# Optimization experiments

Measured on AMD Instinct MI355X. Metric: run time of the kernel, lower is better.

## Reference

```python
import jax, jax.numpy as jnp
import numpy as np

N, C, H, W = 4, 256, 64, 64
C_EMBED = C // 2  # 128

def setup_inputs() -> dict:
    key = jax.random.key(0)
    k1, k2, k3, k4 = jax.random.split(key, 4)
    x = jax.random.normal(k1, (N, C, H, W), dtype=jnp.float32)
    # 1x1 conv weights stored as [out_ch, in_ch] (torch Conv2d weight squeezed)
    theta_w = jax.random.normal(k2, (C_EMBED, C), dtype=jnp.float32) * 0.01
    phi_w = jax.random.normal(k3, (C_EMBED, C), dtype=jnp.float32) * 0.01
    proj_w = jax.random.normal(k4, (C, C), dtype=jnp.float32) * 0.01
    return {"x": x, "theta_w": theta_w, "phi_w": phi_w, "proj_w": proj_w}

def reference(x, theta_w, phi_w, proj_w):
    n, c, h, w = x.shape
    s = h * w
    xf = x.reshape(n, c, s)  # [n, c, s]
    theta = jnp.einsum('ec,ncs->nse', theta_w, xf)  # [n, s, e]
    phi = jnp.einsum('ec,ncs->nes', phi_w, xf)      # [n, e, s]
    scale = jnp.sqrt(jnp.float32(theta_w.shape[0]))
    f = jnp.einsum('nse,net->nst', theta, phi) / scale  # [n, s, s]
    f = jax.nn.softmax(f, axis=-1)
    y = jnp.einsum('nst,nct->ncs', f, xf)  # attend over g = x, -> [n, c, s]
    res = jnp.einsum('oc,ncs->nos', proj_w, y)  # 1x1 projection conv
    return x + res.reshape(n, c, h, w)
```

## Files before the change

kernel.cpp:

```cpp
#include <hip/hip_runtime.h>
#include <cstdint>
#include <cstddef>

#define NB 4
#define CH 256
#define SS 4096
#define EE 128
#define QSCALE 0.08838834764831845f

typedef __attribute__((ext_vector_type(8))) short bfrag;
typedef __attribute__((ext_vector_type(8))) unsigned short u16x8;
typedef __attribute__((ext_vector_type(4))) float f32x4;

__device__ __forceinline__ unsigned short f2bf(float f) {
  union { float f; unsigned int u; } v; v.f = f;
  unsigned int u = v.u;
  unsigned int r = u + 0x7FFFu + ((u >> 16) & 1u);
  return (unsigned short)(r >> 16);
}

__device__ __forceinline__ void lds_barrier() {
  asm volatile("s_waitcnt lgkmcnt(0)" ::: "memory");
  __builtin_amdgcn_s_barrier();
}

__global__ __launch_bounds__(256) void cvt_w(
    const float* __restrict__ thw, const float* __restrict__ phw,
    const float* __restrict__ pw,
    unsigned short* __restrict__ thwb, unsigned short* __restrict__ phwb,
    unsigned short* __restrict__ pwb)
{
  const int nw4 = EE * CH / 4;
  const int np4 = CH * CH / 4;
  int i = blockIdx.x * 256 + threadIdx.x;
  const float* src; unsigned short* dst; int off;
  if      (i < nw4)           { src = thw; dst = thwb; off = i; }
  else if (i < 2 * nw4)       { src = phw; dst = phwb; off = i - nw4; }
  else if (i < 2 * nw4 + np4) { src = pw;  dst = pwb;  off = i - 2 * nw4; }
  else return;
  float4 v = reinterpret_cast<const float4*>(src)[off];
  ushort4 o;
  o.x = f2bf(v.x); o.y = f2bf(v.y); o.z = f2bf(v.z); o.w = f2bf(v.w);
  reinterpret_cast<ushort4*>(dst)[off] = o;
}

__global__ __launch_bounds__(512) void pass1_qk(
    const float* __restrict__ x,
    const unsigned short* __restrict__ thw,
    const unsigned short* __restrict__ phw,
    unsigned short* __restrict__ xb,
    unsigned short* __restrict__ Qt,
    unsigned short* __restrict__ Kt)
{
  __shared__ unsigned short xT[64][CH + 8];
  const int t  = threadIdx.x;
  const int n  = blockIdx.y;
  const int s0 = blockIdx.x * 64;

  {
    const int soff = (t & 15) * 4;
    const int c0   = t >> 4;
    #pragma unroll
    for (int ci = 0; ci < 8; ++ci) {
      const int c = c0 + ci * 32;
      const size_t rowoff = ((size_t)n * CH + c) * SS + s0;
      float4 v = reinterpret_cast<const float4*>(x + rowoff)[soff >> 2];
      ushort4 o;
      o.x = f2bf(v.x); o.y = f2bf(v.y); o.z = f2bf(v.z); o.w = f2bf(v.w);
      reinterpret_cast<ushort4*>(xb + rowoff)[soff >> 2] = o;
      xT[soff + 0][c] = o.x;
      xT[soff + 1][c] = o.y;
      xT[soff + 2][c] = o.z;
      xT[soff + 3][c] = o.w;
    }
  }
  __syncthreads();

  const int w    = t >> 6;
  const int lane = t & 63;
  const int q    = lane >> 4;
  const int mr   = lane & 15;
  const int wrow = (w & 3) * 16;
  const int half = w >> 2;

  bfrag a[8];
  {
    const bfrag* rp = reinterpret_cast<const bfrag*>(&xT[wrow + mr][0]);
    #pragma unroll
    for (int k = 0; k < 8; ++k) a[k] = rp[k * 4 + q];
  }

  const unsigned short* wsel = half ? phw : thw;
  unsigned short*       osel = half ? Kt  : Qt;
  const float           sc   = half ? 1.0f : QSCALE;
  const bfrag* wp = reinterpret_cast<const bfrag*>(wsel);
  #pragma unroll
  for (int nt = 0; nt < 8; ++nt) {
    f32x4 acc = {0.f, 0.f, 0.f, 0.f};
    #pragma unroll
    for (int k = 0; k < 8; ++k) {
      bfrag b = wp[(nt * 16 + mr) * (CH / 8) + k * 4 + q];
      acc = __builtin_amdgcn_mfma_f32_16x16x32_bf16(a[k], b, acc, 0, 0, 0);
    }
    #pragma unroll
    for (int i = 0; i < 4; ++i) {
      const int srow = s0 + wrow + q * 4 + i;
      osel[((size_t)n * SS + srow) * EE + nt * 16 + mr] = f2bf(acc[i] * sc);
    }
  }
}

__global__ __launch_bounds__(512, 2) void pass2_attn(
    const unsigned short* __restrict__ Qt,
    const unsigned short* __restrict__ Kt,
    const unsigned short* __restrict__ xb,
    const unsigned short* __restrict__ pwb,
    const float* __restrict__ x,
    float* __restrict__ out)
{
  __shared__ __align__(16) unsigned char SMEM[51968];
  float          (*S_lds)[132] = reinterpret_cast<float(*)[132]>(SMEM);
  unsigned short (*P_lds)[136] = reinterpret_cast<unsigned short(*)[136]>(SMEM + 33792);
  float* row_m     = reinterpret_cast<float*>(SMEM + 51200);
  float* row_l     = reinterpret_cast<float*>(SMEM + 51456);
  float* row_alpha = reinterpret_cast<float*>(SMEM + 51712);

  const int t    = threadIdx.x;
  const int id   = blockIdx.x;
  const int xcd  = id & 7;
  const int n    = xcd >> 1;
  const int s0   = ((id >> 3) * 2 + (xcd & 1)) * 64;
  const int w    = t >> 6;
  const int lane = t & 63;
  const int q    = lane >> 4;
  const int mr   = lane & 15;

  if (t < 64) { row_m[t] = -INFINITY; row_l[t] = 0.f; }

  bfrag qa[4][4];
  #pragma unroll
  for (int ms = 0; ms < 4; ++ms) {
    const bfrag* rp = reinterpret_cast<const bfrag*>(
        Qt + ((size_t)n * SS + s0 + ms * 16 + mr) * EE);
    #pragma unroll
    for (int k = 0; k < 4; ++k) qa[ms][k] = rp[k * 4 + q];
  }

  f32x4 o_acc[4][2];
  #pragma unroll
  for (int ms = 0; ms < 4; ++ms)
    #pragma unroll
    for (int nt = 0; nt < 2; ++nt) o_acc[ms][nt] = (f32x4){0.f, 0.f, 0.f, 0.f};

  bfrag kb[4];
  {
    const bfrag* rp = reinterpret_cast<const bfrag*>(
        Kt + ((size_t)n * SS + w * 16 + mr) * EE);
    #pragma unroll
    for (int k = 0; k < 4; ++k) kb[k] = rp[k * 4 + q];
  }

  for (int t0 = 0; t0 < SS; t0 += 128) {
    bfrag vb[4][2];
    #pragma unroll
    for (int nt = 0; nt < 2; ++nt) {
      const int c = w * 32 + nt * 16 + mr;
      const bfrag* vp = reinterpret_cast<const bfrag*>(
          xb + ((size_t)n * CH + c) * SS + t0);
      #pragma unroll
      for (int kk = 0; kk < 4; ++kk) vb[kk][nt] = vp[kk * 4 + q];
    }

    #pragma unroll
    for (int ms = 0; ms < 4; ++ms) {
      f32x4 acc = {0.f, 0.f, 0.f, 0.f};
      #pragma unroll
      for (int k = 0; k < 4; ++k)
        acc = __builtin_amdgcn_mfma_f32_16x16x32_bf16(qa[ms][k], kb[k], acc, 0, 0, 0);
      #pragma unroll
      for (int i = 0; i < 4; ++i)
        S_lds[ms * 16 + q * 4 + i][w * 16 + mr] = acc[i];
    }
    lds_barrier();

    {
      const int t1 = t0 + 128;
      if (t1 < SS) {
        const bfrag* rp = reinterpret_cast<const bfrag*>(
            Kt + ((size_t)n * SS + t1 + w * 16 + mr) * EE);
        #pragma unroll
        for (int k = 0; k < 4; ++k) kb[k] = rp[k * 4 + q];
      }
    }

    {
      const int r  = t >> 3;
      const int cg = t & 7;
      const float4* srow = reinterpret_cast<const float4*>(&S_lds[r][cg * 16]);
      float4 v0 = srow[0], v1 = srow[1], v2 = srow[2], v3 = srow[3];
      float vmax = fmaxf(fmaxf(fmaxf(v0.x, v0.y), fmaxf(v0.z, v0.w)),
                         fmaxf(fmaxf(v1.x, v1.y), fmaxf(v1.z, v1.w)));
      vmax = fmaxf(vmax, fmaxf(fmaxf(fmaxf(v2.x, v2.y), fmaxf(v2.z, v2.w)),
                               fmaxf(fmaxf(v3.x, v3.y), fmaxf(v3.z, v3.w))));
      vmax = fmaxf(vmax, __shfl_xor(vmax, 1, 8));
      vmax = fmaxf(vmax, __shfl_xor(vmax, 2, 8));
      vmax = fmaxf(vmax, __shfl_xor(vmax, 4, 8));
      const float m_old = row_m[r];
      const float m_new = fmaxf(m_old, vmax);

      float p[16];
      p[0]=__expf(v0.x-m_new); p[1]=__expf(v0.y-m_new); p[2]=__expf(v0.z-m_new); p[3]=__expf(v0.w-m_new);
      p[4]=__expf(v1.x-m_new); p[5]=__expf(v1.y-m_new); p[6]=__expf(v1.z-m_new); p[7]=__expf(v1.w-m_new);
      p[8]=__expf(v2.x-m_new); p[9]=__expf(v2.y-m_new); p[10]=__expf(v2.z-m_new); p[11]=__expf(v2.w-m_new);
      p[12]=__expf(v3.x-m_new); p[13]=__expf(v3.y-m_new); p[14]=__expf(v3.z-m_new); p[15]=__expf(v3.w-m_new);
      float sum = 0.f;
      u16x8 pk0, pk1;
      #pragma unroll
      for (int j = 0; j < 8; ++j) { sum += p[j];     pk0[j] = f2bf(p[j]); }
      #pragma unroll
      for (int j = 0; j < 8; ++j) { sum += p[8 + j]; pk1[j] = f2bf(p[8 + j]); }
      *reinterpret_cast<u16x8*>(&P_lds[r][cg * 16])     = pk0;
      *reinterpret_cast<u16x8*>(&P_lds[r][cg * 16 + 8]) = pk1;
      sum += __shfl_xor(sum, 1, 8);
      sum += __shfl_xor(sum, 2, 8);
      sum += __shfl_xor(sum, 4, 8);
      if (cg == 0) {
        const float al = __expf(m_old - m_new);
        row_alpha[r] = al;
        row_m[r]     = m_new;
        row_l[r]     = row_l[r] * al + sum;
      }
    }
    lds_barrier();

    #pragma unroll
    for (int ms = 0; ms < 4; ++ms) {
      float al[4];
      #pragma unroll
      for (int i = 0; i < 4; ++i) al[i] = row_alpha[ms * 16 + q * 4 + i];
      #pragma unroll
      for (int nt = 0; nt < 2; ++nt)
        #pragma unroll
        for (int i = 0; i < 4; ++i) o_acc[ms][nt][i] *= al[i];
    }

    #pragma unroll
    for (int kk = 0; kk < 4; ++kk) {
      bfrag pa[4];
      #pragma unroll
      for (int ms = 0; ms < 4; ++ms)
        pa[ms] = reinterpret_cast<const bfrag*>(&P_lds[ms * 16 + mr][0])[kk * 4 + q];
      #pragma unroll
      for (int nt = 0; nt < 2; ++nt)
        #pragma unroll
        for (int ms = 0; ms < 4; ++ms)
          o_acc[ms][nt] = __builtin_amdgcn_mfma_f32_16x16x32_bf16(
              pa[ms], vb[kk][nt], o_acc[ms][nt], 0, 0, 0);
    }
  }

  __syncthreads();
  unsigned short (*Y_lds)[CH + 8] =
      reinterpret_cast<unsigned short(*)[CH + 8]>(SMEM);

  #pragma unroll
  for (int ms = 0; ms < 4; ++ms) {
    float inv[4];
    #pragma unroll
    for (int i = 0; i < 4; ++i) inv[i] = 1.0f / row_l[ms * 16 + q * 4 + i];
    #pragma unroll
    for (int nt = 0; nt < 2; ++nt) {
      const int c = w * 32 + nt * 16 + mr;
      #pragma unroll
      for (int i = 0; i < 4; ++i)
        Y_lds[ms * 16 + q * 4 + i][c] = f2bf(o_acc[ms][nt][i] * inv[i]);
    }
  }
  __syncthreads();

  #pragma unroll
  for (int ot = 0; ot < 2; ++ot) {
    const int o0 = w * 32 + ot * 16;
    bfrag a[8];
    {
      const bfrag* ap = reinterpret_cast<const bfrag*>(pwb + (o0 + mr) * CH);
      #pragma unroll
      for (int k = 0; k < 8; ++k) a[k] = ap[k * 4 + q];
    }
    #pragma unroll
    for (int st = 0; st < 4; ++st) {
      f32x4 acc = {0.f, 0.f, 0.f, 0.f};
      const bfrag* bp = reinterpret_cast<const bfrag*>(&Y_lds[st * 16 + mr][0]);
      #pragma unroll
      for (int k = 0; k < 8; ++k)
        acc = __builtin_amdgcn_mfma_f32_16x16x32_bf16(a[k], bp[k * 4 + q], acc, 0, 0, 0);
      #pragma unroll
      for (int i = 0; i < 4; ++i) {
        const int o = o0 + q * 4 + i;
        const int s = s0 + st * 16 + mr;
        const size_t idx = ((size_t)n * CH + o) * SS + s;
        out[idx] = x[idx] + acc[i];
      }
    }
  }
}

extern "C" void kernel_launch(void* const* d_in, const int* in_sizes, int n_in,
                              void* d_out, int out_size, void* d_ws, size_t ws_size,
                              hipStream_t stream) {
  const float* x   = (const float*)d_in[0];
  const float* thw = (const float*)d_in[1];
  const float* phw = (const float*)d_in[2];
  const float* pw  = (const float*)d_in[3];
  float* out = (float*)d_out;

  unsigned short* xb   = (unsigned short*)d_ws;
  unsigned short* Qt   = xb + (size_t)NB * CH * SS;
  unsigned short* Kt   = Qt + (size_t)NB * SS * EE;
  unsigned short* thwb = Kt + (size_t)NB * SS * EE;
  unsigned short* phwb = thwb + EE * CH;
  unsigned short* pwb  = phwb + EE * CH;

  const int nw4 = EE * CH / 4;
  const int np4 = CH * CH / 4;
  const int totw4 = 2 * nw4 + np4;
  cvt_w<<<(totw4 + 255) / 256, 256, 0, stream>>>(thw, phw, pw, thwb, phwb, pwb);

  pass1_qk  <<<dim3(SS / 64, NB), 512, 0, stream>>>(x, thwb, phwb, xb, Qt, Kt);
  pass2_attn<<<dim3(NB * SS / 64), 512, 0, stream>>>(Qt, Kt, xb, pwb, x, out);
}
```

Measured before the change: 195.8 us.

## Split attention along the key dimension with separate merge and projection kernel

Replaces the single fused attention-plus-projection kernel with a split-K flash-attention pass. It uses 128-query tiles, each block covering half of the keys, and writes partial outputs plus max and sum statistics to workspace. A second kernel merges the two halves with softmax rescaling and then applies the 1x1 projection and the residual. The goal is more work per block and better reuse of Q held in LDS, at the cost of extra global traffic for the partials, a larger LDS footprint, and an extra launch. The old fused path remains as a fallback when the workspace is too small.

```diff
diff --git a/kernel.cpp b/kernel.cpp
--- a/kernel.cpp
+++ b/kernel.cpp
@@ -10,6 +10,7 @@
 
 typedef __attribute__((ext_vector_type(8))) short bfrag;
 typedef __attribute__((ext_vector_type(8))) unsigned short u16x8;
+typedef __attribute__((ext_vector_type(8))) _Float16 h16x8;
 typedef __attribute__((ext_vector_type(4))) float f32x4;
 
 __device__ __forceinline__ unsigned short f2bf(float f) {
@@ -110,7 +111,311 @@
   }
 }
 
-__global__ __launch_bounds__(512, 2) void pass2_attn(
+__global__ __launch_bounds__(512, 2) void pass2a(
+    const unsigned short* __restrict__ Qt,
+    const unsigned short* __restrict__ Kt,
+    const unsigned short* __restrict__ xb,
+    void* __restrict__ Opart_,
+    float* __restrict__ ML,
+    int use32)
+{
+  __shared__ __align__(16) unsigned char SMEM[138752];
+  float          (*S_lds)[132] = reinterpret_cast<float(*)[132]>(SMEM);
+  unsigned short (*P_lds)[136] = reinterpret_cast<unsigned short(*)[136]>(SMEM + 67584);
+  unsigned short (*Q_lds)[136] = reinterpret_cast<unsigned short(*)[136]>(SMEM + 102400);
+  float* row_m     = reinterpret_cast<float*>(SMEM + 137216);
+  float* row_l     = reinterpret_cast<float*>(SMEM + 137728);
+  float* row_alpha = reinterpret_cast<float*>(SMEM + 138240);
+
+  float*    Of32 = reinterpret_cast<float*>(Opart_);
+  _Float16* Oh16 = reinterpret_cast<_Float16*>(Opart_);
+
+  const int t     = threadIdx.x;
+  const int id    = blockIdx.x;
+  const int xcd   = id & 7;
+  const int n     = xcd >> 1;
+  const int h     = xcd & 1;
+  const int qt    = id >> 3;
+  const int s0    = qt * 128;
+  const int kbase = h * 2048;
+
+  const int w    = t >> 6;
+  const int lane = t & 63;
+  const int q    = lane >> 4;
+  const int mr   = lane & 15;
+
+  if (t < 128) { row_m[t] = -INFINITY; row_l[t] = 0.f; }
+
+  {
+    const int col = (t & 15) * 8;
+    #pragma unroll
+    for (int j = 0; j < 4; ++j) {
+      const int row = (t >> 4) + j * 32;
+      *reinterpret_cast<u16x8*>(&Q_lds[row][col]) =
+          *reinterpret_cast<const u16x8*>(
+              Qt + ((size_t)n * SS + s0 + row) * EE + col);
+    }
+  }
+
+  f32x4 o_accA[4][2], o_accB[4][2];
+  #pragma unroll
+  for (int ms = 0; ms < 4; ++ms)
+    #pragma unroll
+    for (int nt = 0; nt < 2; ++nt) {
+      o_accA[ms][nt] = (f32x4){0.f, 0.f, 0.f, 0.f};
+      o_accB[ms][nt] = (f32x4){0.f, 0.f, 0.f, 0.f};
+    }
+
+  __syncthreads();
+
+  bfrag kb[4];
+  {
+    const bfrag* rp = reinterpret_cast<const bfrag*>(
+        Kt + ((size_t)n * SS + kbase + w * 16 + mr) * EE);
+    #pragma unroll
+    for (int k = 0; k < 4; ++k) kb[k] = rp[k * 4 + q];
+  }
+
+#define QK_HALF(RB)                                                          \
+  do {                                                                       \
+    _Pragma("unroll")                                                        \
+    for (int ms = 0; ms < 4; ++ms) {                                         \
+      f32x4 acc = {0.f, 0.f, 0.f, 0.f};                                      \
+      _Pragma("unroll")                                                      \
+      for (int k = 0; k < 4; ++k) {                                          \
+        bfrag aq = *reinterpret_cast<const bfrag*>(                          \
+            &Q_lds[(RB) + ms * 16 + mr][(k * 4 + q) * 8]);                   \
+        acc = __builtin_amdgcn_mfma_f32_16x16x32_bf16(aq, kb[k], acc, 0,0,0);\
+      }                                                                      \
+      _Pragma("unroll")                                                      \
+      for (int i = 0; i < 4; ++i)                                            \
+        S_lds[(RB) + ms * 16 + q * 4 + i][w * 16 + mr] = acc[i];             \
+    }                                                                        \
+  } while (0)
+
+#define PV_HALF(OACC, RB)                                                    \
+  do {                                                                       \
+    _Pragma("unroll")                                                        \
+    for (int ms = 0; ms < 4; ++ms) {                                         \
+      float al[4];                                                           \
+      _Pragma("unroll")                                                      \
+      for (int i = 0; i < 4; ++i) al[i] = row_alpha[(RB) + ms*16 + q*4 + i]; \
+      _Pragma("unroll")                                                      \
+      for (int nt = 0; nt < 2; ++nt)                                         \
+        _Pragma("unroll")                                                    \
+        for (int i = 0; i < 4; ++i) OACC[ms][nt][i] *= al[i];                \
+    }                                                                        \
+    _Pragma("unroll")                                                        \
+    for (int kk = 0; kk < 4; ++kk) {                                         \
+      bfrag pa[4];                                                           \
+      _Pragma("unroll")                                                      \
+      for (int ms = 0; ms < 4; ++ms)                                         \
+        pa[ms] = reinterpret_cast<const bfrag*>(                             \
+            &P_lds[(RB) + ms * 16 + mr][0])[kk * 4 + q];                     \
+      _Pragma("unroll")                                                      \
+      for (int nt = 0; nt < 2; ++nt)                                         \
+        _Pragma("unroll")                                                    \
+        for (int ms = 0; ms < 4; ++ms)                                       \
+          OACC[ms][nt] = __builtin_amdgcn_mfma_f32_16x16x32_bf16(            \
+              pa[ms], vb[kk][nt], OACC[ms][nt], 0, 0, 0);                    \
+    }                                                                        \
+  } while (0)
+
+  for (int t0 = 0; t0 < 2048; t0 += 128) {
+    bfrag vb[4][2];
+    #pragma unroll
+    for (int nt = 0; nt < 2; ++nt) {
+      const int c = w * 32 + nt * 16 + mr;
+      const bfrag* vp = reinterpret_cast<const bfrag*>(
+          xb + ((size_t)n * CH + c) * SS + kbase + t0);
+      #pragma unroll
+      for (int kk = 0; kk < 4; ++kk) vb[kk][nt] = vp[kk * 4 + q];
+    }
+
+    QK_HALF(0);
+    QK_HALF(64);
+    lds_barrier();
+
+    if (t0 + 128 < 2048) {
+      const bfrag* rp = reinterpret_cast<const bfrag*>(
+          Kt + ((size_t)n * SS + kbase + t0 + 128 + w * 16 + mr) * EE);
+      #pragma unroll
+      for (int k = 0; k < 4; ++k) kb[k] = rp[k * 4 + q];
+    }
+
+    #pragma unroll
+    for (int sh = 0; sh < 2; ++sh) {
+      const int r  = sh * 64 + (t >> 3);
+      const int cg = t & 7;
+      const float4* srow = reinterpret_cast<const float4*>(&S_lds[r][cg * 16]);
+      float4 v0 = srow[0], v1 = srow[1], v2 = srow[2], v3 = srow[3];
+      float vmax = fmaxf(fmaxf(fmaxf(v0.x, v0.y), fmaxf(v0.z, v0.w)),
+                         fmaxf(fmaxf(v1.x, v1.y), fmaxf(v1.z, v1.w)));
+      vmax = fmaxf(vmax, fmaxf(fmaxf(fmaxf(v2.x, v2.y), fmaxf(v2.z, v2.w)),
+                               fmaxf(fmaxf(v3.x, v3.y), fmaxf(v3.z, v3.w))));
+      vmax = fmaxf(vmax, __shfl_xor(vmax, 1, 8));
+      vmax = fmaxf(vmax, __shfl_xor(vmax, 2, 8));
+      vmax = fmaxf(vmax, __shfl_xor(vmax, 4, 8));
+      const float m_old = row_m[r];
+      const float m_new = fmaxf(m_old, vmax);
+
+      float p[16];
+      p[0]=__expf(v0.x-m_new); p[1]=__expf(v0.y-m_new); p[2]=__expf(v0.z-m_new); p[3]=__expf(v0.w-m_new);
+      p[4]=__expf(v1.x-m_new); p[5]=__expf(v1.y-m_new); p[6]=__expf(v1.z-m_new); p[7]=__expf(v1.w-m_new);
+      p[8]=__expf(v2.x-m_new); p[9]=__expf(v2.y-m_new); p[10]=__expf(v2.z-m_new); p[11]=__expf(v2.w-m_new);
+      p[12]=__expf(v3.x-m_new); p[13]=__expf(v3.y-m_new); p[14]=__expf(v3.z-m_new); p[15]=__expf(v3.w-m_new);
+      float sum = 0.f;
+      u16x8 pk0, pk1;
+      #pragma unroll
+      for (int j = 0; j < 8; ++j) { sum += p[j];     pk0[j] = f2bf(p[j]); }
+      #pragma unroll
+      for (int j = 0; j < 8; ++j) { sum += p[8 + j]; pk1[j] = f2bf(p[8 + j]); }
+      *reinterpret_cast<u16x8*>(&P_lds[r][cg * 16])     = pk0;
+      *reinterpret_cast<u16x8*>(&P_lds[r][cg * 16 + 8]) = pk1;
+      sum += __shfl_xor(sum, 1, 8);
+      sum += __shfl_xor(sum, 2, 8);
+      sum += __shfl_xor(sum, 4, 8);
+      if (cg == 0) {
+        const float al = __expf(m_old - m_new);
+        row_alpha[r] = al;
+        row_m[r]     = m_new;
+        row_l[r]     = row_l[r] * al + sum;
+      }
+    }
+    lds_barrier();
+
+    PV_HALF(o_accA, 0);
+    PV_HALF(o_accB, 64);
+  }
+
+  const size_t p = ((size_t)(n * 32 + qt)) * 2 + h;
+
+#define EPI_HALF(OACC, RB)                                                   \
+  do {                                                                       \
+    _Pragma("unroll")                                                        \
+    for (int ms = 0; ms < 4; ++ms) {                                         \
+      float inv[4];                                                          \
+      _Pragma("unroll")                                                      \
+      for (int i = 0; i < 4; ++i)                                            \
+        inv[i] = 1.0f / row_l[(RB) + ms * 16 + q * 4 + i];                   \
+      _Pragma("unroll")                                                      \
+      for (int nt = 0; nt < 2; ++nt)                                         \
+        _Pragma("unroll")                                                    \
+        for (int i = 0; i < 4; ++i) {                                        \
+          const size_t oi =                                                  \
+              (p * 128 + (RB) + ms * 16 + q * 4 + i) * 256 +                 \
+              w * 32 + nt * 16 + mr;                                         \
+          const float yv = OACC[ms][nt][i] * inv[i];                         \
+          if (use32) Of32[oi] = yv; else Oh16[oi] = (_Float16)yv;            \
+        }                                                                    \
+    }                                                                        \
+  } while (0)
+
+  EPI_HALF(o_accA, 0);
+  EPI_HALF(o_accB, 64);
+  if (t < 128) {
+    ML[p * 256 + t * 2]     = row_m[t];
+    ML[p * 256 + t * 2 + 1] = row_l[t];
+  }
+}
+
+__global__ __launch_bounds__(512) void pass2b(
+    const void* __restrict__ Opart_,
+    const float* __restrict__ ML,
+    const unsigned short* __restrict__ pwb,
+    const float* __restrict__ x,
+    float* __restrict__ out,
+    int use32)
+{
+  __shared__ __align__(16) unsigned char SMEM[34816];
+  unsigned short (*Y_lds)[CH + 8] =
+      reinterpret_cast<unsigned short(*)[CH + 8]>(SMEM);
+  float* w0 = reinterpret_cast<float*>(SMEM + 33792);
+  float* w1 = reinterpret_cast<float*>(SMEM + 34048);
+
+  const float*    Of32 = reinterpret_cast<const float*>(Opart_);
+  const _Float16* Oh16 = reinterpret_cast<const _Float16*>(Opart_);
+
+  const int t   = threadIdx.x;
+  const int id  = blockIdx.x;
+  const int n   = id >> 6;
+  const int sub = id & 63;
+  const int s0  = sub * 64;
+  const int qt  = sub >> 1;
+  const int rb  = (sub & 1) * 64;
+  const size_t p0 = ((size_t)(n * 32 + qt)) * 2;
+
+  if (t < 64) {
+    const float ma = ML[p0 * 256 + (rb + t) * 2];
+    const float la = ML[p0 * 256 + (rb + t) * 2 + 1];
+    const float mb = ML[(p0 + 1) * 256 + (rb + t) * 2];
+    const float lb = ML[(p0 + 1) * 256 + (rb + t) * 2 + 1];
+    const float m  = fmaxf(ma, mb);
+    const float e0 = __expf(ma - m) * la;
+    const float e1 = __expf(mb - m) * lb;
+    const float iL = 1.0f / (e0 + e1);
+    w0[t] = e0 * iL;
+    w1[t] = e1 * iL;
+  }
+  __syncthreads();
+
+  {
+    const int r = t >> 3;
+    #pragma unroll
+    for (int seg = 0; seg < 4; ++seg) {
+      const int c0 = (t & 7) * 8 + seg * 64;
+      const size_t ai = (p0 * 128 + rb + r) * 256 + c0;
+      const size_t bi = ((p0 + 1) * 128 + rb + r) * 256 + c0;
+      float fa[8], fb[8];
+      if (use32) {
+        #pragma unroll
+        for (int j = 0; j < 8; ++j) { fa[j] = Of32[ai + j]; fb[j] = Of32[bi + j]; }
+      } else {
+        h16x8 ha = *reinterpret_cast<const h16x8*>(Oh16 + ai);
+        h16x8 hb = *reinterpret_cast<const h16x8*>(Oh16 + bi);
+        #pragma unroll
+        for (int j = 0; j < 8; ++j) { fa[j] = (float)ha[j]; fb[j] = (float)hb[j]; }
+      }
+      u16x8 y;
+      #pragma unroll
+      for (int j = 0; j < 8; ++j) y[j] = f2bf(fa[j] * w0[r] + fb[j] * w1[r]);
+      *reinterpret_cast<u16x8*>(&Y_lds[r][c0]) = y;
+    }
+  }
+  __syncthreads();
+
+  const int w    = t >> 6;
+  const int lane = t & 63;
+  const int q    = lane >> 4;
+  const int mr   = lane & 15;
+  #pragma unroll
+  for (int ot = 0; ot < 2; ++ot) {
+    const int o0 = w * 32 + ot * 16;
+    bfrag a[8];
+    {
+      const bfrag* ap = reinterpret_cast<const bfrag*>(pwb + (o0 + mr) * CH);
+      #pragma unroll
+      for (int k = 0; k < 8; ++k) a[k] = ap[k * 4 + q];
+    }
+    #pragma unroll
+    for (int st = 0; st < 4; ++st) {
+      f32x4 acc = {0.f, 0.f, 0.f, 0.f};
+      const bfrag* bp = reinterpret_cast<const bfrag*>(&Y_lds[st * 16 + mr][0]);
+      #pragma unroll
+      for (int k = 0; k < 8; ++k)
+        acc = __builtin_amdgcn_mfma_f32_16x16x32_bf16(a[k], bp[k * 4 + q], acc, 0, 0, 0);
+      #pragma unroll
+      for (int i = 0; i < 4; ++i) {
+        const int o = o0 + q * 4 + i;
+        const int s = s0 + st * 16 + mr;
+        const size_t idx = ((size_t)n * CH + o) * SS + s;
+        out[idx] = x[idx] + acc[i];
+      }
+    }
+  }
+}
+
+__global__ __launch_bounds__(512, 2) void pass2_full(
     const unsigned short* __restrict__ Qt,
     const unsigned short* __restrict__ Kt,
     const unsigned short* __restrict__ xb,
@@ -320,12 +625,26 @@
   unsigned short* thwb = Kt + (size_t)NB * SS * EE;
   unsigned short* phwb = thwb + EE * CH;
   unsigned short* pwb  = phwb + EE * CH;
+  float*          ML   = (float*)(pwb + CH * CH);
+  void*           Opart = (void*)(ML + (size_t)256 * 128 * 2);
+
+  const size_t opart_off = (size_t)((char*)Opart - (char*)d_ws);
+  const size_t opart_elems = (size_t)256 * 128 * 256;
+  const int fits32 = ws_size >= opart_off + opart_elems * 4;
+  const int fits16 = ws_size >= opart_off + opart_elems * 2;
 
   const int nw4 = EE * CH / 4;
   const int np4 = CH * CH / 4;
   const int totw4 = 2 * nw4 + np4;
   cvt_w<<<(totw4 + 255) / 256, 256, 0, stream>>>(thw, phw, pw, thwb, phwb, pwb);
 
-  pass1_qk  <<<dim3(SS / 64, NB), 512, 0, stream>>>(x, thwb, phwb, xb, Qt, Kt);
-  pass2_attn<<<dim3(NB * SS / 64), 512, 0, stream>>>(Qt, Kt, xb, pwb, x, out);
-}
+  pass1_qk<<<dim3(SS / 64, NB), 512, 0, stream>>>(x, thwb, phwb, xb, Qt, Kt);
+
+  if (fits32 || fits16) {
+    const int use32 = fits32 ? 1 : 0;
+    pass2a<<<dim3(256), 512, 0, stream>>>(Qt, Kt, xb, Opart, ML, use32);
+    pass2b<<<dim3(256), 512, 0, stream>>>(Opart, ML, pwb, x, out, use32);
+  } else {
+    pass2_full<<<dim3(NB * SS / 64), 512, 0, stream>>>(Qt, Kt, xb, pwb, x, out);
+  }
+}
```

Measured after the change: 190.5 us. -2.7%, faster.
